# Performance work log

Hardware: AMD Instinct MI355X
Metric: run time of the kernel (lower is better)

Reference implementation:

```python
import jax, jax.numpy as jnp
import numpy as np

NUM_CLASSES = 1000
B, Q, N = 64, 900, 30
NO_OBJ_W = 0.1
COST_CLASS, COST_BBOX, COST_GIOU = 1.0, 5.0, 2.0
LOSS_BBOX, LOSS_GIOU = 5.0, 2.0


def cxcywh_to_xyxy(b):
    cx, cy, w, h = b[..., 0], b[..., 1], b[..., 2], b[..., 3]
    return jnp.stack([cx - 0.5 * w, cy - 0.5 * h, cx + 0.5 * w, cy + 0.5 * h], axis=-1)


def _area(b):
    return jnp.clip(b[..., 2] - b[..., 0], 0.0) * jnp.clip(b[..., 3] - b[..., 1], 0.0)


def giou_xyxy(b1, b2):
    # GIoU over broadcastable [..., 4] xyxy boxes
    lt = jnp.maximum(b1[..., :2], b2[..., :2])
    rb = jnp.minimum(b1[..., 2:], b2[..., 2:])
    wh = jnp.clip(rb - lt, 0.0)
    inter = wh[..., 0] * wh[..., 1]
    union = _area(b1) + _area(b2) - inter
    iou = inter / jnp.maximum(union, 1e-6)
    ltc = jnp.minimum(b1[..., :2], b2[..., :2])
    rbc = jnp.maximum(b1[..., 2:], b2[..., 2:])
    whc = jnp.clip(rbc - ltc, 0.0)
    ac = whc[..., 0] * whc[..., 1]
    return iou - (ac - union) / jnp.maximum(ac, 1e-6)


def _cost_matrices(pred_logits, pred_boxes, tgt_labels, tgt_boxes_xyxy):
    prob = jax.nn.softmax(pred_logits, axis=-1)                    # [B,Q,C+1]
    cost_cls = -jax.vmap(lambda p, l: p[:, l])(prob, tgt_labels)   # [B,Q,N]
    pred_xyxy = jnp.clip(cxcywh_to_xyxy(pred_boxes), 0.0, 1.0)     # [B,Q,4]
    cost_l1 = jnp.sum(jnp.abs(pred_xyxy[:, :, None] - tgt_boxes_xyxy[:, None]), -1)
    cost_g = -giou_xyxy(pred_xyxy[:, :, None], tgt_boxes_xyxy[:, None])
    C = COST_CLASS * cost_cls + COST_BBOX * cost_l1 + COST_GIOU * cost_g
    return C, pred_xyxy


def greedy_match(C):
    # faithful to the module's torch fallback matcher: iteratively pick the
    # global minimum of the cost matrix, masking used rows/cols (host-side,
    # non-differentiable, exactly like the detach->cpu->assignment in torch)
    Cw = C.copy()
    Qn, Nn = Cw.shape
    rows, cols = [], []
    for _ in range(min(Qn, Nn)):
        i = int(np.argmin(Cw))
        pi, ti = divmod(i, Nn)
        rows.append(pi)
        cols.append(ti)
        Cw[pi, :] = 1e9
        Cw[:, ti] = 1e9
    return np.array(rows, dtype=np.int32), np.array(cols, dtype=np.int32)


def match_all(Cnp):
    pis, tis = zip(*[greedy_match(Cnp[b]) for b in range(Cnp.shape[0])])
    return jnp.asarray(np.stack(pis)), jnp.asarray(np.stack(tis))  # [B,N] each


def set_losses(pred_logits, pred_xyxy, tgt_labels, tgt_boxes_xyxy, pi, ti):
    ce_weight = jnp.ones(NUM_CLASSES + 1, jnp.float32).at[NUM_CLASSES].set(NO_OBJ_W)
    bidx = jnp.arange(B)[:, None]
    # target class per query: matched -> tgt label, else no-object class
    tc = jnp.full((B, Q), NUM_CLASSES, dtype=jnp.int32)
    tc = tc.at[bidx, pi].set(jnp.take_along_axis(tgt_labels, ti, axis=1))
    nll = -jnp.take_along_axis(jax.nn.log_softmax(pred_logits, -1), tc[..., None].astype(jnp.int32), axis=2)[..., 0]
    w = ce_weight[tc]
    ce = jnp.mean(jnp.sum(w * nll, axis=1) / jnp.sum(w, axis=1))  # torch weighted CE mean, per image
    p_m = pred_xyxy[bidx, pi]          # [B,N,4] matched preds
    t_m = tgt_boxes_xyxy[bidx, ti]     # [B,N,4] matched targets
    l1 = jnp.mean(jnp.mean(jnp.abs(p_m - t_m), axis=(1, 2)))
    gl = jnp.mean(jnp.mean(1.0 - giou_xyxy(p_m, t_m), axis=1))
    total = ce + LOSS_BBOX * l1 + LOSS_GIOU * gl
    return jnp.stack([total, ce, l1, gl])


def setup_inputs():
    key = jax.random.key(0)
    k1, k2, k3, k4, k5 = jax.random.split(key, 5)
    pred_logits = jax.random.normal(k1, (B, Q, NUM_CLASSES + 1), jnp.float32)
    pred_boxes = jax.random.uniform(k2, (B, Q, 4), jnp.float32, 0.05, 0.95)
    tgt_labels = jax.random.randint(k3, (B, N), 0, NUM_CLASSES, dtype=jnp.int32)
    lt = jax.random.uniform(k4, (B, N, 2), jnp.float32, 0.0, 0.6)
    wh = jax.random.uniform(k5, (B, N, 2), jnp.float32, 0.02, 0.37)
    tgt_boxes_xyxy = jnp.concatenate([lt, lt + wh], axis=-1)  # valid 0..1 xyxy
    return {"pred_logits": pred_logits, "pred_boxes": pred_boxes,
            "tgt_labels": tgt_labels, "tgt_boxes_xyxy": tgt_boxes_xyxy}


def reference(pred_logits, pred_boxes, tgt_labels, tgt_boxes_xyxy):
    C, pred_xyxy = _cost_matrices(pred_logits, pred_boxes, tgt_labels, tgt_boxes_xyxy)
    pi, ti = match_all(np.asarray(jax.lax.stop_gradient(C)))
    # returns [loss_total, loss_ce, loss_bbox, loss_giou]
    return set_losses(pred_logits, pred_xyxy, tgt_labels, tgt_boxes_xyxy, pi, ti)
```

## Files before the change

kernel.cpp:

```cpp
#include <hip/hip_runtime.h>
#include <math.h>

#define BB 64
#define QQ 900
#define NN 30
#define C1 1001
#define QN (QQ * NN)
#define NO_OBJ_W 0.1f

__device__ unsigned g_ord[BB * QN];
__device__ unsigned long long g_top[BB * NN * NN];
__device__ float  g_logZ[BB * QQ];
__device__ float  g_noobj[BB * QQ];
__device__ float4 g_xyxy[BB * QQ];
__device__ float  g_acc[3];
__device__ unsigned g_cnt;

__device__ __forceinline__ float giou_f(float ax1, float ay1, float ax2, float ay2,
                                        float bx1, float by1, float bx2, float by2) {
    float ix1 = fmaxf(ax1, bx1), iy1 = fmaxf(ay1, by1);
    float ix2 = fminf(ax2, bx2), iy2 = fminf(ay2, by2);
    float iw = fmaxf(ix2 - ix1, 0.f), ih = fmaxf(iy2 - iy1, 0.f);
    float inter = iw * ih;
    float areaA = fmaxf(ax2 - ax1, 0.f) * fmaxf(ay2 - ay1, 0.f);
    float areaB = fmaxf(bx2 - bx1, 0.f) * fmaxf(by2 - by1, 0.f);
    float uni = areaA + areaB - inter;
    float iou = inter / fmaxf(uni, 1e-6f);
    float cx1 = fminf(ax1, bx1), cy1 = fminf(ay1, by1);
    float cx2 = fmaxf(ax2, bx2), cy2 = fmaxf(ay2, by2);
    float cw = fmaxf(cx2 - cx1, 0.f), ch = fmaxf(cy2 - cy1, 0.f);
    float ac = cw * ch;
    return iou - (ac - uni) / fmaxf(ac, 1e-6f);
}

__device__ __forceinline__ unsigned ord_map(float f) {
    unsigned u = __float_as_uint(f);
    return (u & 0x80000000u) ? ~u : (u | 0x80000000u);
}

__global__ __launch_bounds__(256) void cost_kernel(const float* __restrict__ logits,
                                                   const float* __restrict__ pboxes,
                                                   const int*   __restrict__ labels,
                                                   const float* __restrict__ tboxes) {
    if (blockIdx.x == 0 && threadIdx.x == 0) {
        g_acc[0] = 0.f; g_acc[1] = 0.f; g_acc[2] = 0.f;
        g_cnt = 0u;
    }
    int gwave = (blockIdx.x * blockDim.x + threadIdx.x) >> 6;
    int lane = threadIdx.x & 63;
    if (gwave >= BB * QQ) return;
    int b = gwave / QQ;

    size_t s = (size_t)gwave * C1;
    size_t a0 = (s + 3) >> 2;
    size_t a1 = (s + C1) >> 2;
    int nq = (int)(a1 - a0);
    int hh = (int)(a0 * 4 - s);
    int tt = (int)((s + C1) - a1 * 4);
    const float4* L4 = (const float4*)logits;

    float4 v4[4];
#pragma unroll
    for (int i = 0; i < 4; ++i) {
        int qq = lane + 64 * i;
        v4[i] = (qq < nq) ? L4[a0 + qq]
                          : make_float4(-INFINITY, -INFINITY, -INFINITY, -INFINITY);
    }
    float e1 = (lane < hh) ? logits[s + lane] : -INFINITY;
    float e2 = (lane < tt) ? logits[a1 * 4 + lane] : -INFINITY;

    float mx = fmaxf(e1, e2);
#pragma unroll
    for (int i = 0; i < 4; ++i)
        mx = fmaxf(mx, fmaxf(fmaxf(v4[i].x, v4[i].y), fmaxf(v4[i].z, v4[i].w)));
#pragma unroll
    for (int off = 32; off; off >>= 1) mx = fmaxf(mx, __shfl_xor(mx, off));

    float sm = __expf(e1 - mx) + __expf(e2 - mx);
#pragma unroll
    for (int i = 0; i < 4; ++i) {
        sm += __expf(v4[i].x - mx);
        sm += __expf(v4[i].y - mx);
        sm += __expf(v4[i].z - mx);
        sm += __expf(v4[i].w - mx);
    }
#pragma unroll
    for (int off = 32; off; off >>= 1) sm += __shfl_xor(sm, off);
    float logZ = mx + __logf(sm);

    float row1000 = logits[s + 1000];

    const float* pb = pboxes + (size_t)gwave * 4;
    float cx = pb[0], cy = pb[1], w = pb[2], h = pb[3];
    float x1 = fminf(fmaxf(cx - 0.5f * w, 0.f), 1.f);
    float y1 = fminf(fmaxf(cy - 0.5f * h, 0.f), 1.f);
    float x2 = fminf(fmaxf(cx + 0.5f * w, 0.f), 1.f);
    float y2 = fminf(fmaxf(cy + 0.5f * h, 0.f), 1.f);

    if (lane == 0) {
        g_logZ[gwave] = logZ;
        g_noobj[gwave] = logZ - row1000;
        g_xyxy[gwave] = make_float4(x1, y1, x2, y2);
    }

    if (lane < NN) {
        int t = lane;
        int lab = labels[b * NN + t];
        float pcls = __expf(logits[s + lab] - logZ);
        const float* tb = tboxes + ((size_t)(b * NN + t)) * 4;
        float tx1 = tb[0], ty1 = tb[1], tx2 = tb[2], ty2 = tb[3];
        float l1 = fabsf(x1 - tx1) + fabsf(y1 - ty1) + fabsf(x2 - tx2) + fabsf(y2 - ty2);
        float g = giou_f(x1, y1, x2, y2, tx1, ty1, tx2, ty2);
        g_ord[(size_t)gwave * NN + t] = ord_map(-pcls + 5.0f * l1 - 2.0f * g);
    }
}

__global__ __launch_bounds__(256) void select_kernel() {
    int gw = (blockIdx.x * blockDim.x + threadIdx.x) >> 6;
    int lane = threadIdx.x & 63;
    if (gw >= BB * NN) return;
    int b = gw / NN;
    int t = gw - b * NN;

    unsigned long long key[16];
    if (lane < 60) {
#pragma unroll
        for (int j = 0; j < 15; ++j) {
            int q = j * 60 + lane;
            unsigned o = g_ord[((size_t)(b * QQ + q)) * NN + t];
            key[j] = ((unsigned long long)o << 32) | (unsigned)(q * NN + t);
        }
    } else {
#pragma unroll
        for (int j = 0; j < 15; ++j) key[j] = ~0ull;
    }
    key[15] = ~0ull;

#pragma unroll
    for (int kk = 2; kk <= 16; kk <<= 1) {
#pragma unroll
        for (int jj = kk >> 1; jj > 0; jj >>= 1) {
#pragma unroll
            for (int i = 0; i < 16; ++i) {
                int l = i ^ jj;
                if (l > i) {
                    bool up = ((i & kk) == 0);
                    unsigned long long a = key[i], c = key[l];
                    bool sw = up ? (a > c) : (a < c);
                    key[i] = sw ? c : a;
                    key[l] = sw ? a : c;
                }
            }
        }
    }

    unsigned long long* outp = g_top + (size_t)gw * NN;
    for (int it = 0; it < NN; ++it) {
        unsigned long long m = key[0];
#pragma unroll
        for (int off = 32; off; off >>= 1) {
            unsigned long long o = __shfl_xor(m, off);
            m = (o < m) ? o : m;
        }
        if (lane == it) outp[it] = m;
        if (key[0] == m) {
#pragma unroll
            for (int j = 0; j < 15; ++j) key[j] = key[j + 1];
            key[15] = ~0ull;
        }
    }
}

__global__ __launch_bounds__(256) void match_loss_kernel(const float* __restrict__ logits,
                                                         const int*   __restrict__ labels,
                                                         const float* __restrict__ tboxes,
                                                         float* __restrict__ out) {
    int b = blockIdx.x;
    int tid = threadIdx.x;

    __shared__ unsigned long long s_cand[NN * NN];
    __shared__ int s_pi[NN], s_ti[NN];
    __shared__ unsigned s_dead[29];
    __shared__ float s4[4][4];

    const unsigned long long* topb = g_top + (size_t)b * NN * NN;
    for (int i = tid; i < NN * NN; i += 256) s_cand[i] = topb[i];
    if (tid < 29) s_dead[tid] = 0u;
    __syncthreads();

    if (tid < 64) {
        int lane = tid;
        bool colLive = lane < NN;
        int ptr = 0;
        unsigned long long cand = colLive ? s_cand[lane * NN] : ~0ull;
        unsigned rowc = colLive ? ((unsigned)cand) / NN : 0u;

        for (int it = 0; it < NN; ++it) {
            unsigned long long g = colLive ? cand : ~0ull;
#pragma unroll
            for (int off = 32; off; off >>= 1) {
                unsigned long long o = __shfl_xor(g, off);
                g = (o < g) ? o : g;
            }
            unsigned e = (unsigned)g;
            int pq = e / NN;
            int pt = e - pq * NN;
            if (lane == 0) {
                s_pi[it] = pq;
                s_ti[it] = pt;
                s_dead[pq >> 5] |= (1u << (pq & 31));
            }
            if (lane == pt) colLive = false;
            if (colLive && rowc == (unsigned)pq) {
                do {
                    ++ptr;
                    cand = s_cand[lane * NN + ptr];
                    rowc = ((unsigned)cand) / NN;
                } while ((s_dead[rowc >> 5] >> (rowc & 31)) & 1u);
            }
        }
    }
    __syncthreads();

    float sA = 0.f;
    for (int q = tid; q < QQ; q += 256) sA += g_noobj[b * QQ + q];

    float sB = 0.f, sL = 0.f, sG = 0.f;
    if (tid < NN) {
        int pq = s_pi[tid], pt = s_ti[tid];
        int gq = b * QQ + pq;
        int lab = labels[b * NN + pt];
        float mnll = g_logZ[gq] - logits[(size_t)gq * C1 + lab];
        sB = mnll - NO_OBJ_W * g_noobj[gq];
        float4 p = g_xyxy[gq];
        const float* tb = tboxes + ((size_t)(b * NN + pt)) * 4;
        float tx1 = tb[0], ty1 = tb[1], tx2 = tb[2], ty2 = tb[3];
        sL = fabsf(p.x - tx1) + fabsf(p.y - ty1) + fabsf(p.z - tx2) + fabsf(p.w - ty2);
        sG = 1.0f - giou_f(p.x, p.y, p.z, p.w, tx1, ty1, tx2, ty2);
    }

    int lane = tid & 63, wid = tid >> 6;
    float vv[4] = {sA, sB, sL, sG};
#pragma unroll
    for (int j = 0; j < 4; ++j) {
        float x = vv[j];
#pragma unroll
        for (int off = 32; off; off >>= 1) x += __shfl_xor(x, off);
        if (lane == 0) s4[wid][j] = x;
    }
    __syncthreads();
    if (tid == 0) {
        float a = 0.f, bs = 0.f, l = 0.f, g = 0.f;
        for (int w = 0; w < 4; ++w) { a += s4[w][0]; bs += s4[w][1]; l += s4[w][2]; g += s4[w][3]; }
        atomicAdd(&g_acc[0], NO_OBJ_W * a + bs);
        atomicAdd(&g_acc[1], l);
        atomicAdd(&g_acc[2], g);
        __threadfence();
        unsigned prev = atomicAdd(&g_cnt, 1u);
        if (prev == BB - 1) {
            __threadfence();
            float ce = atomicAdd(&g_acc[0], 0.f) / (float)(BB * 117);
            float l1 = atomicAdd(&g_acc[1], 0.f) / (float)(BB * NN * 4);
            float gl = atomicAdd(&g_acc[2], 0.f) / (float)(BB * NN);
            out[0] = ce + 5.0f * l1 + 2.0f * gl;
            out[1] = ce;
            out[2] = l1;
            out[3] = gl;
        }
    }
}

extern "C" void kernel_launch(void* const* d_in, const int* in_sizes, int n_in,
                              void* d_out, int out_size, void* d_ws, size_t ws_size,
                              hipStream_t stream) {
    const float* pred_logits = (const float*)d_in[0];
    const float* pred_boxes  = (const float*)d_in[1];
    const int*   tgt_labels  = (const int*)d_in[2];
    const float* tgt_boxes   = (const float*)d_in[3];
    float* out = (float*)d_out;

    cost_kernel<<<(BB * QQ) / 4, 256, 0, stream>>>(pred_logits, pred_boxes, tgt_labels, tgt_boxes);
    select_kernel<<<(BB * NN) / 4, 256, 0, stream>>>();
    match_loss_kernel<<<BB, 256, 0, stream>>>(pred_logits, tgt_labels, tgt_boxes, out);
}
```

Baseline: 96.62 us.

## Extract two minima per wave reduction in top-k and greedy matching loops

The per-warp top-30 extraction now runs a combined min/second-min butterfly reduction, so it takes 15 rounds of shuffles instead of 30. The greedy matching loop also computes the two smallest column candidates and accepts both in one iteration when they share no row or column. This halves the serial count of shuffle reductions on the critical path, at the cost of twice the shuffles per round and extra compare logic. Correctness of accepting the second minimum relies on it staying the global minimum once the first pick's row and column are removed; the column-pointer advance only handles candidates invalidated by those picks.

```diff
diff --git a/kernel.cpp b/kernel.cpp
--- a/kernel.cpp
+++ b/kernel.cpp
@@ -155,15 +155,28 @@
     }
 
     unsigned long long* outp = g_top + (size_t)gw * NN;
-    for (int it = 0; it < NN; ++it) {
-        unsigned long long m = key[0];
+#pragma unroll 1
+    for (int r = 0; r < NN / 2; ++r) {
+        unsigned long long m1 = key[0];
+        unsigned long long m2 = key[1];
 #pragma unroll
         for (int off = 32; off; off >>= 1) {
-            unsigned long long o = __shfl_xor(m, off);
-            m = (o < m) ? o : m;
-        }
-        if (lane == it) outp[it] = m;
-        if (key[0] == m) {
+            unsigned long long o1 = __shfl_xor(m1, off);
+            unsigned long long o2 = __shfl_xor(m2, off);
+            unsigned long long lo = (o1 < m1) ? o1 : m1;
+            unsigned long long hi = (o1 < m1) ? m1 : o1;
+            unsigned long long n2 = (o2 < m2) ? o2 : m2;
+            m1 = lo;
+            m2 = (hi < n2) ? hi : n2;
+        }
+        if (lane == 2 * r)     outp[2 * r]     = m1;
+        if (lane == 2 * r + 1) outp[2 * r + 1] = m2;
+        if (key[0] == m1 || key[0] == m2) {
+#pragma unroll
+            for (int j = 0; j < 15; ++j) key[j] = key[j + 1];
+            key[15] = ~0ull;
+        }
+        if (key[0] == m2) {
 #pragma unroll
             for (int j = 0; j < 15; ++j) key[j] = key[j + 1];
             key[15] = ~0ull;
@@ -195,29 +208,46 @@
         unsigned long long cand = colLive ? s_cand[lane * NN] : ~0ull;
         unsigned rowc = colLive ? ((unsigned)cand) / NN : 0u;
 
-        for (int it = 0; it < NN; ++it) {
-            unsigned long long g = colLive ? cand : ~0ull;
+        int it = 0;
+        while (it < NN) {
+            unsigned long long m1 = colLive ? cand : ~0ull;
+            unsigned long long m2 = ~0ull;
 #pragma unroll
             for (int off = 32; off; off >>= 1) {
-                unsigned long long o = __shfl_xor(g, off);
-                g = (o < g) ? o : g;
+                unsigned long long o1 = __shfl_xor(m1, off);
+                unsigned long long o2 = __shfl_xor(m2, off);
+                unsigned long long lo = (o1 < m1) ? o1 : m1;
+                unsigned long long hi = (o1 < m1) ? m1 : o1;
+                unsigned long long n2 = (o2 < m2) ? o2 : m2;
+                m1 = lo;
+                m2 = (hi < n2) ? hi : n2;
             }
-            unsigned e = (unsigned)g;
-            int pq = e / NN;
-            int pt = e - pq * NN;
+            unsigned e1 = (unsigned)m1;
+            int q1 = e1 / NN, t1 = e1 - (e1 / NN) * NN;
+            unsigned e2 = (unsigned)m2;
+            int q2 = e2 / NN, t2 = e2 - (e2 / NN) * NN;
+            bool acc2 = (m2 != ~0ull) && (it + 1 < NN) && (q2 != q1) && (t2 != t1);
+
             if (lane == 0) {
-                s_pi[it] = pq;
-                s_ti[it] = pt;
-                s_dead[pq >> 5] |= (1u << (pq & 31));
+                s_pi[it] = q1;
+                s_ti[it] = t1;
+                s_dead[q1 >> 5] |= (1u << (q1 & 31));
+                if (acc2) {
+                    s_pi[it + 1] = q2;
+                    s_ti[it + 1] = t2;
+                    s_dead[q2 >> 5] |= (1u << (q2 & 31));
+                }
             }
-            if (lane == pt) colLive = false;
-            if (colLive && rowc == (unsigned)pq) {
+            if (lane == t1) colLive = false;
+            if (acc2 && lane == t2) colLive = false;
+            if (colLive && (rowc == (unsigned)q1 || (acc2 && rowc == (unsigned)q2))) {
                 do {
                     ++ptr;
                     cand = s_cand[lane * NN + ptr];
                     rowc = ((unsigned)cand) / NN;
                 } while ((s_dead[rowc >> 5] >> (rowc & 31)) & 1u);
             }
+            it += acc2 ? 2 : 1;
         }
     }
     __syncthreads();
```

Measured after the change: 94.44 us. 1.02x faster.
